# Kernel optimization log

Measured on AMD Instinct MI355X. Metric: run time of the kernel, lower is better.

## Reference

```python
import jax, jax.numpy as jnp
import numpy as np

M_DIM = 32          # vec_dim m
L1 = L2 = L3 = L4 = 3
L_TOT = L1 * L2 * L3 * L4   # 81
R = 2               # rank1..rank4 window size
B_SZ = 4
D_SZ = 16           # D1 = D2 = D3 = D4


def _make_bbasis():
    # Bbasis[idx, i] = prod_k cos(2*pi*(j_k+1)/(i+2)), idx = flattened (j1,j2,j3,j4)
    i = jnp.arange(M_DIM, dtype=jnp.float32)
    def c(Lk):
        j = jnp.arange(Lk, dtype=jnp.float32)
        return jnp.cos(2.0 * jnp.pi * (j[:, None] + 1.0) / (i[None, :] + 2.0))  # [Lk, m]
    c1, c2, c3, c4 = c(L1), c(L2), c(L3), c(L4)
    Bb = (c1[:, None, None, None, :] * c2[None, :, None, None, :]
          * c3[None, None, :, None, :] * c4[None, None, None, :, :])
    return Bb.reshape(L_TOT, M_DIM)


def _window_basis_idx(n1, n2, n3, n4):
    # linear mode, drop: window top-left coords are 0..n_k-1 with step 1
    j1 = jnp.arange(n1) % L1
    j2 = jnp.arange(n2) % L2
    j3 = jnp.arange(n3) % L3
    j4 = jnp.arange(n4) % L4
    idx = (((j1[:, None, None, None] * L2 + j2[None, :, None, None]) * L3
            + j3[None, None, :, None]) * L4 + j4[None, None, None, :])
    return idx.reshape(-1)  # [n_windows]


def setup_inputs() -> dict:
    key = jax.random.key(0)
    k1, k2, k3 = jax.random.split(key, 3)
    arr_batch = jax.random.normal(k1, (B_SZ, D_SZ, D_SZ, D_SZ, D_SZ, M_DIM), dtype=jnp.float32)
    # M initialized near identity (nn.init.eye_ + perturbation so grads are non-trivial)
    M = jnp.eye(M_DIM, dtype=jnp.float32) + 0.01 * jax.random.normal(k2, (M_DIM, M_DIM), dtype=jnp.float32)
    # Acoeff ~ U(-0.1, 0.1) as in reset_parameters
    Acoeff = jax.random.uniform(k3, (M_DIM, L_TOT), dtype=jnp.float32, minval=-0.1, maxval=0.1)
    Bbasis = _make_bbasis()  # fixed buffer, computed deterministically
    return {"arr_batch": arr_batch, "M": M, "Acoeff": Acoeff, "Bbasis": Bbasis}


def reference(arr_batch, M, Acoeff, Bbasis):
    Bsz, D1, D2, D3, D4, m = arr_batch.shape
    # map every vector through M (x @ M.T); avg-pooling commutes with the linear map,
    # matching `mapped = windows @ M.T` then mean over the window
    mapped = jnp.einsum('bpqrsm,nm->bpqrsn', arr_batch, M)
    # 4D sliding window (rank=2 per dim, stride 1, 'drop' -> VALID), rank_op='avg'
    win = (1, R, R, R, R, 1)
    agg = jax.lax.reduce_window(mapped, 0.0, jax.lax.add, win, (1,) * 6, 'VALID') / float(R ** 4)
    n1, n2, n3, n4 = agg.shape[1:5]
    n_win = n1 * n2 * n3 * n4
    agg = agg.reshape(Bsz, n_win, m)            # [B, W, m]
    idx = _window_basis_idx(n1, n2, n3, n4)     # [W]
    phi = Bbasis[idx]                           # [W, m]
    # t_k = Acoeff[:, j_k] * (Bbasis[j_k, :] . agg_k); representation = mean_k t_k
    s = jnp.einsum('bwm,wm->bw', agg, phi)      # [B, W]
    t = s[:, :, None] * Acoeff.T[idx][None]     # [B, W, m]
    return t.mean(axis=1)                       # [B, m]
```

## Files before the change

kernel.cpp:

```cpp
#include <hip/hip_runtime.h>


static __device__ __forceinline__ void add4(float4& a, const float4& b) {
    a.x += b.x; a.y += b.y; a.z += b.z; a.w += b.w;
}
static __device__ __forceinline__ void fma4(float4& a, float w, const float4& b) {
    a.x = fmaf(w, b.x, a.x); a.y = fmaf(w, b.y, a.y);
    a.z = fmaf(w, b.z, a.z); a.w = fmaf(w, b.w, a.w);
}

__global__ __launch_bounds__(128) void sdd4_prep(
    const float* __restrict__ Mmat,
    const float* __restrict__ Bbasis,
    float* __restrict__ G,
    float* __restrict__ out)
{
    __shared__ float M_lds[32 * 33];
    const int t  = threadIdx.x;
    const int bx = blockIdx.x;

    const float4* M4 = reinterpret_cast<const float4*>(Mmat);
    for (int i = t; i < 256; i += 128) {
        float4 v = M4[i];
        float* dst = &M_lds[(i >> 3) * 33 + (i & 7) * 4];
        dst[0] = v.x; dst[1] = v.y; dst[2] = v.z; dst[3] = v.w;
    }
    if (bx == 0 && t < 128) out[t] = 0.0f;
    __syncthreads();

    const int base = bx * 648;
    for (int k = 0; k < 6; ++k) {
        const int o = base + t + k * 128;
        if (o < base + 648) {
            const int jf = o >> 5, m = o & 31;
            const float4* Br = reinterpret_cast<const float4*>(Bbasis + jf * 32);
            float acc = 0.f;
            #pragma unroll
            for (int nv = 0; nv < 8; ++nv) {
                float4 bv = Br[nv];
                acc = fmaf(bv.x, M_lds[(nv * 4 + 0) * 33 + m], acc);
                acc = fmaf(bv.y, M_lds[(nv * 4 + 1) * 33 + m], acc);
                acc = fmaf(bv.z, M_lds[(nv * 4 + 2) * 33 + m], acc);
                acc = fmaf(bv.w, M_lds[(nv * 4 + 3) * 33 + m], acc);
            }
            G[o] = acc;
        }
    }
}

__global__ __launch_bounds__(128) void sdd4_main(
    const float* __restrict__ arr,
    const float* __restrict__ G,
    const float* __restrict__ Acoeff,
    float* __restrict__ out)
{
    __shared__ float4 U_lds[400];
    __shared__ float  V_lds[9 * 33];
    __shared__ float  G_lds[81 * 33];
    __shared__ float  A_lds[81 * 33];
    __shared__ float  c_lds[40];
    __shared__ int    jf_lds[40];

    const int t  = threadIdx.x;
    const int bx = blockIdx.x;
    const int b  = bx >> 8;
    const int p  = (bx >> 4) & 15;
    const int q  = bx & 15;

    const float4* G4 = reinterpret_cast<const float4*>(G);
    for (int i = t; i < 648; i += 128) {
        float4 v = G4[i];
        float* dst = &G_lds[(i >> 3) * 33 + (i & 7) * 4];
        dst[0] = v.x; dst[1] = v.y; dst[2] = v.z; dst[3] = v.w;
    }
    if (t < 81) {
        #pragma unroll
        for (int n = 0; n < 32; ++n)
            A_lds[t * 33 + n] = Acoeff[n * 81 + t];
    }

    const int r  = t >> 3;
    const int mv = t & 7;
    const float4* A4 = reinterpret_cast<const float4*>(arr);
    const size_t tile = (size_t)((b * 16 + p) * 16 + q) * 2048;

    float4 u0 = make_float4(0.f, 0.f, 0.f, 0.f), u1 = u0, u2 = u0;
    #pragma unroll
    for (int s = 0; s < 16; ++s) {
        float4 x = A4[tile + (size_t)(r * 16 + s) * 8 + mv];
        if ((0x36DBu >> s) & 1) add4(u0, x);
        if ((0x6DB6u >> s) & 1) add4(u1, x);
        if ((0xDB6Cu >> s) & 1) add4(u2, x);
    }
    U_lds[r * 25 +      mv] = u0;
    U_lds[r * 25 +  8 + mv] = u1;
    U_lds[r * 25 + 16 + mv] = u2;
    __syncthreads();

    if (t < 72) {
        const int j3  = t / 24;
        const int rem = t % 24;
        const int j4  = rem >> 3;
        const int mv2 = rem & 7;
        const unsigned msk = (j3 == 0) ? 0x36DBu : (j3 == 1 ? 0x6DB6u : 0xDB6Cu);
        float4 acc = make_float4(0.f, 0.f, 0.f, 0.f);
        #pragma unroll
        for (int rr = 0; rr < 16; ++rr) {
            float w = (float)((msk >> rr) & 1u);
            fma4(acc, w, U_lds[rr * 25 + j4 * 8 + mv2]);
        }
        const int jj = j3 * 3 + j4;
        float* dv = &V_lds[jj * 33 + mv2 * 4];
        dv[0] = acc.x; dv[1] = acc.y; dv[2] = acc.z; dv[3] = acc.w;
    }
    __syncthreads();

    int l1_0, l1_1 = 0, n1;
    if      (p == 0)  { l1_0 = 0; n1 = 1; }
    else if (p == 15) { l1_0 = 2; n1 = 1; }
    else              { l1_0 = (p - 1) % 3; l1_1 = p % 3; n1 = 2; }
    int l2_0, l2_1 = 0, n2;
    if      (q == 0)  { l2_0 = 0; n2 = 1; }
    else if (q == 15) { l2_0 = 2; n2 = 1; }
    else              { l2_0 = (q - 1) % 3; l2_1 = q % 3; n2 = 2; }

    const int ncomb = n1 * n2 * 9;
    if (t < ncomb) {
        const int jj  = t % 9;
        const int c12 = t / 9;
        const int i1idx = (n2 == 2) ? (c12 >> 1) : c12;
        const int i2idx = (n2 == 2) ? (c12 & 1)  : 0;
        const int i1 = i1idx ? l1_1 : l1_0;
        const int i2 = i2idx ? l2_1 : l2_0;
        const int jf = (i1 * 3 + i2) * 9 + jj;
        float acc = 0.f;
        #pragma unroll
        for (int m = 0; m < 32; ++m)
            acc = fmaf(G_lds[jf * 33 + m], V_lds[jj * 33 + m], acc);
        c_lds[t]  = acc;
        jf_lds[t] = jf;
    }
    __syncthreads();

    if (t < 32) {
        float acc = 0.f;
        for (int k = 0; k < ncomb; ++k)
            acc = fmaf(A_lds[jf_lds[k] * 33 + t], c_lds[k], acc);
        atomicAdd(&out[b * 32 + t], acc * (1.0f / 810000.0f));
    }
}

extern "C" void kernel_launch(void* const* d_in, const int* in_sizes, int n_in,
                              void* d_out, int out_size, void* d_ws, size_t ws_size,
                              hipStream_t stream) {
    const float* arr    = (const float*)d_in[0];
    const float* Mmat   = (const float*)d_in[1];
    const float* Acoeff = (const float*)d_in[2];
    const float* Bbasis = (const float*)d_in[3];
    float* G = (float*)d_ws;

    sdd4_prep<<<dim3(4),    dim3(128), 0, stream>>>(Mmat, Bbasis, G, (float*)d_out);
    sdd4_main<<<dim3(1024), dim3(128), 0, stream>>>(arr, G, Acoeff, (float*)d_out);
}
```

Before: 90.36 us.

## Double threads per block, issue tile loads early, copy Acoeff with vector loads

Doubles the main kernel's block to 256 threads so each thread loads 8 instead of 16 float4 values of the input tile, and issues all of those loads before the G and Acoeff staging so more memory requests are in flight. The Acoeff staging becomes a straight float4 copy that keeps its original layout instead of a strided transposing scalar loop. The second-stage reduction now skips masked terms and sums two half-partials per row. This costs more LDS for the U buffer and more registers per thread, which may reduce occupancy.

```diff
diff --git a/kernel.cpp b/kernel.cpp
--- a/kernel.cpp
+++ b/kernel.cpp
@@ -3,10 +3,6 @@
 
 static __device__ __forceinline__ void add4(float4& a, const float4& b) {
     a.x += b.x; a.y += b.y; a.z += b.z; a.w += b.w;
-}
-static __device__ __forceinline__ void fma4(float4& a, float w, const float4& b) {
-    a.x = fmaf(w, b.x, a.x); a.y = fmaf(w, b.y, a.y);
-    a.z = fmaf(w, b.z, a.z); a.w = fmaf(w, b.w, a.w);
 }
 
 __global__ __launch_bounds__(128) void sdd4_prep(
@@ -48,16 +44,16 @@
     }
 }
 
-__global__ __launch_bounds__(128) void sdd4_main(
+__global__ __launch_bounds__(256) void sdd4_main(
     const float* __restrict__ arr,
     const float* __restrict__ G,
     const float* __restrict__ Acoeff,
     float* __restrict__ out)
 {
-    __shared__ float4 U_lds[400];
+    __shared__ float4 U_lds[800];
     __shared__ float  V_lds[9 * 33];
     __shared__ float  G_lds[81 * 33];
-    __shared__ float  A_lds[81 * 33];
+    __shared__ __align__(16) float A_lds[32 * 81];
     __shared__ float  c_lds[40];
     __shared__ int    jf_lds[40];
 
@@ -67,34 +63,42 @@
     const int p  = (bx >> 4) & 15;
     const int q  = bx & 15;
 
+    const int mv = t & 7;
+    const int h  = (t >> 3) & 1;
+    const int r  = t >> 4;
+
+    const float4* A4 = reinterpret_cast<const float4*>(arr);
+    const size_t tile = (size_t)((b * 16 + p) * 16 + q) * 2048;
+    float4 x[8];
+    #pragma unroll
+    for (int i = 0; i < 8; ++i)
+        x[i] = A4[tile + (size_t)((r * 16 + h * 8 + i) * 8 + mv)];
+
     const float4* G4 = reinterpret_cast<const float4*>(G);
-    for (int i = t; i < 648; i += 128) {
+    for (int i = t; i < 648; i += 256) {
         float4 v = G4[i];
         float* dst = &G_lds[(i >> 3) * 33 + (i & 7) * 4];
         dst[0] = v.x; dst[1] = v.y; dst[2] = v.z; dst[3] = v.w;
     }
-    if (t < 81) {
-        #pragma unroll
-        for (int n = 0; n < 32; ++n)
-            A_lds[t * 33 + n] = Acoeff[n * 81 + t];
-    }
-
-    const int r  = t >> 3;
-    const int mv = t & 7;
-    const float4* A4 = reinterpret_cast<const float4*>(arr);
-    const size_t tile = (size_t)((b * 16 + p) * 16 + q) * 2048;
+    const float4* Ac4 = reinterpret_cast<const float4*>(Acoeff);
+    float4* Al4 = reinterpret_cast<float4*>(A_lds);
+    for (int i = t; i < 648; i += 256)
+        Al4[i] = Ac4[i];
 
     float4 u0 = make_float4(0.f, 0.f, 0.f, 0.f), u1 = u0, u2 = u0;
+    const unsigned m0 = 0x36DBu >> (h * 8);
+    const unsigned m1 = 0x6DB6u >> (h * 8);
+    const unsigned m2 = 0xDB6Cu >> (h * 8);
     #pragma unroll
-    for (int s = 0; s < 16; ++s) {
-        float4 x = A4[tile + (size_t)(r * 16 + s) * 8 + mv];
-        if ((0x36DBu >> s) & 1) add4(u0, x);
-        if ((0x6DB6u >> s) & 1) add4(u1, x);
-        if ((0xDB6Cu >> s) & 1) add4(u2, x);
+    for (int i = 0; i < 8; ++i) {
+        if ((m0 >> i) & 1) add4(u0, x[i]);
+        if ((m1 >> i) & 1) add4(u1, x[i]);
+        if ((m2 >> i) & 1) add4(u2, x[i]);
     }
-    U_lds[r * 25 +      mv] = u0;
-    U_lds[r * 25 +  8 + mv] = u1;
-    U_lds[r * 25 + 16 + mv] = u2;
+    const int ub = (r * 2 + h) * 25;
+    U_lds[ub +      mv] = u0;
+    U_lds[ub +  8 + mv] = u1;
+    U_lds[ub + 16 + mv] = u2;
     __syncthreads();
 
     if (t < 72) {
@@ -106,8 +110,10 @@
         float4 acc = make_float4(0.f, 0.f, 0.f, 0.f);
         #pragma unroll
         for (int rr = 0; rr < 16; ++rr) {
-            float w = (float)((msk >> rr) & 1u);
-            fma4(acc, w, U_lds[rr * 25 + j4 * 8 + mv2]);
+            if ((msk >> rr) & 1) {
+                add4(acc, U_lds[(rr * 2 + 0) * 25 + j4 * 8 + mv2]);
+                add4(acc, U_lds[(rr * 2 + 1) * 25 + j4 * 8 + mv2]);
+            }
         }
         const int jj = j3 * 3 + j4;
         float* dv = &V_lds[jj * 33 + mv2 * 4];
@@ -145,7 +151,7 @@
     if (t < 32) {
         float acc = 0.f;
         for (int k = 0; k < ncomb; ++k)
-            acc = fmaf(A_lds[jf_lds[k] * 33 + t], c_lds[k], acc);
+            acc = fmaf(A_lds[t * 81 + jf_lds[k]], c_lds[k], acc);
         atomicAdd(&out[b * 32 + t], acc * (1.0f / 810000.0f));
     }
 }
@@ -160,5 +166,5 @@
     float* G = (float*)d_ws;
 
     sdd4_prep<<<dim3(4),    dim3(128), 0, stream>>>(Mmat, Bbasis, G, (float*)d_out);
-    sdd4_main<<<dim3(1024), dim3(128), 0, stream>>>(arr, G, Acoeff, (float*)d_out);
+    sdd4_main<<<dim3(1024), dim3(256), 0, stream>>>(arr, G, Acoeff, (float*)d_out);
 }
```

After: 88.22 us. 2.4% less time.
